# Optimization experiments

Measured on AMD Instinct MI355X. Metric: run time of the kernel, lower is better.

The kernel has to match this reference:

```python
import jax, jax.numpy as jnp
import numpy as np

PATCH = 16


def setup_inputs() -> dict:
    key = jax.random.key(0)
    x = jax.random.normal(key, (256, 3, 224, 224), dtype=jnp.float32)
    return {"x": x}


def reference(x):
    P = PATCH
    B, C, Hi, Wi = x.shape
    h, w = Hi // P, Wi // P  # grid rows (h) and cols (w)
    # 'b c (h p1) (w p2) -> b w h p1 p2 c'
    patches = x.reshape(B, C, h, P, w, P).transpose(0, 4, 2, 3, 5, 1)  # (B, w, h, p1, p2, C)
    # center_rotate: transpose p1<->p2 for patches with grid col j in [w/3, 2w/3]
    # and grid row k in [h/3, 2h/3] (original skips j < W/3 or j > 2W/3, same for k)
    jw = jnp.arange(w)
    kh = jnp.arange(h)
    mw = (jw >= w / 3) & (jw <= 2 * w / 3)
    mh = (kh >= h / 3) & (kh <= 2 * h / 3)
    mask = (mw[:, None] & mh[None, :])[None, :, :, None, None, None]  # (1, w, h, 1, 1, 1)
    rot = jnp.where(mask, jnp.swapaxes(patches, 3, 4), patches)  # (B, w, h, a3, a4, C)
    # 'b w h p2 p1 c -> b c (h p2) (w p1)': axis3 is read as p2 (inner height),
    # axis4 as p1 (inner width) -- i.e. every patch gets transposed on reassembly,
    # so center patches (transposed twice) come back in original orientation.
    out = rot.transpose(0, 5, 2, 3, 1, 4).reshape(B, C, h * P, w * P)
    return out
```

## Files before the change

kernel.cpp:

```cpp
#include <hip/hip_runtime.h>


#define W4 56
#define IMG_F4 12544
#define LDS_S 84
#define NT 512

__global__ __launch_bounds__(NT) void patch_rotate_kernel(
    const float4* __restrict__ x, float4* __restrict__ out) {
  const int bc = blockIdx.x;
  const float4* __restrict__ xs = x + (size_t)bc * IMG_F4;
  float4* __restrict__ os = out + (size_t)bc * IMG_F4;
  const int tid = threadIdx.x;

  __shared__ float ldsT[5 * 16 * LDS_S];

  for (int i = tid; i < 1600; i += NT) {
    const int sr = i / 20;
    const int c4 = i % 20;
    const float4 v = xs[(80 + sr) * W4 + 20 + c4];
    const int ks = sr >> 4;
    const int ar = sr & 15;
    const int jl = c4 >> 2;
    const int ac0 = (c4 & 3) << 2;
    float* p = ldsT + (ks * 16 + ac0) * LDS_S + jl * 16 + ar;
    p[0 * LDS_S] = v.x;
    p[1 * LDS_S] = v.y;
    p[2 * LDS_S] = v.z;
    p[3 * LDS_S] = v.w;
  }

  for (int i = tid; i < 4480; i += NT) os[i] = xs[i];
  for (int i = 8960 + tid; i < IMG_F4; i += NT) os[i] = xs[i];
  for (int i = tid; i < 2880; i += NT) {
    const int r = i / 36;
    const int cc = i % 36;
    const int c4 = cc < 20 ? cc : cc + 20;
    const int idx = (80 + r) * W4 + c4;
    os[idx] = xs[idx];
  }

  __syncthreads();

  for (int i = tid; i < 1600; i += NT) {
    const int orr = i / 20;
    const int c4 = i % 20;
    const float* p = ldsT + orr * LDS_S + c4 * 4;
    float4 v;
    v.x = p[0]; v.y = p[1]; v.z = p[2]; v.w = p[3];
    os[(80 + orr) * W4 + 20 + c4] = v;
  }
}

extern "C" void kernel_launch(void* const* d_in, const int* in_sizes, int n_in,
                              void* d_out, int out_size, void* d_ws, size_t ws_size,
                              hipStream_t stream) {
  const float* x = (const float*)d_in[0];
  float* out = (float*)d_out;
  patch_rotate_kernel<<<768, NT, 0, stream>>>((const float4*)x, (float4*)out);
}
```

Before: 275.4 us.

## Replace per-image LDS block kernel with flat per-float4 elementwise gather kernel

Drops the one-block-per-image design, which staged the center 5x5 patch region through shared memory. It launches one thread per output float4 instead. Non-center elements are copied with nontemporal vector loads and stores. Center elements gather four strided scalars directly from global memory to perform the transpose. This raises the grid size and removes the barrier and LDS traffic, at the cost of uncoalesced strided reads in the center region and more integer index math per thread.

```diff
diff --git a/kernel.cpp b/kernel.cpp
--- a/kernel.cpp
+++ b/kernel.cpp
@@ -1,54 +1,40 @@
 #include <hip/hip_runtime.h>
 
 
+#define HH 224
+#define WW 224
 #define W4 56
-#define IMG_F4 12544
-#define LDS_S 84
-#define NT 512
 
-__global__ __launch_bounds__(NT) void patch_rotate_kernel(
-    const float4* __restrict__ x, float4* __restrict__ out) {
-  const int bc = blockIdx.x;
-  const float4* __restrict__ xs = x + (size_t)bc * IMG_F4;
-  float4* __restrict__ os = out + (size_t)bc * IMG_F4;
-  const int tid = threadIdx.x;
+typedef float vf4 __attribute__((ext_vector_type(4)));
 
-  __shared__ float ldsT[5 * 16 * LDS_S];
+__global__ __launch_bounds__(256) void patch_rotate_kernel(
+    const float* __restrict__ x, float* __restrict__ out, int n4) {
+  int idx = blockIdx.x * blockDim.x + threadIdx.x;
+  if (idx >= n4) return;
 
-  for (int i = tid; i < 1600; i += NT) {
-    const int sr = i / 20;
-    const int c4 = i % 20;
-    const float4 v = xs[(80 + sr) * W4 + 20 + c4];
-    const int ks = sr >> 4;
-    const int ar = sr & 15;
-    const int jl = c4 >> 2;
-    const int ac0 = (c4 & 3) << 2;
-    float* p = ldsT + (ks * 16 + ac0) * LDS_S + jl * 16 + ar;
-    p[0 * LDS_S] = v.x;
-    p[1 * LDS_S] = v.y;
-    p[2 * LDS_S] = v.z;
-    p[3 * LDS_S] = v.w;
-  }
+  int bc   = idx / (HH * W4);
+  int rem  = idx % (HH * W4);
+  int row  = rem / W4;
+  int col4 = rem % W4;
 
-  for (int i = tid; i < 4480; i += NT) os[i] = xs[i];
-  for (int i = 8960 + tid; i < IMG_F4; i += NT) os[i] = xs[i];
-  for (int i = tid; i < 2880; i += NT) {
-    const int r = i / 36;
-    const int cc = i % 36;
-    const int c4 = cc < 20 ? cc : cc + 20;
-    const int idx = (80 + r) * W4 + c4;
-    os[idx] = xs[idx];
-  }
+  int k = row >> 4;
+  int j = col4 >> 2;
 
-  __syncthreads();
+  bool center = (j >= 5) & (j <= 9) & (k >= 5) & (k <= 9);
 
-  for (int i = tid; i < 1600; i += NT) {
-    const int orr = i / 20;
-    const int c4 = i % 20;
-    const float* p = ldsT + orr * LDS_S + c4 * 4;
-    float4 v;
-    v.x = p[0]; v.y = p[1]; v.z = p[2]; v.w = p[3];
-    os[(80 + orr) * W4 + 20 + c4] = v;
+  if (!center) {
+    vf4 v = __builtin_nontemporal_load((const vf4*)x + idx);
+    __builtin_nontemporal_store(v, (vf4*)out + idx);
+  } else {
+    int a3  = row & 15;
+    int a4b = (col4 & 3) << 2;
+    int base = (bc * HH + (k << 4)) * WW + (j << 4) + a3;
+    vf4 v;
+    v.x = x[base + (a4b + 0) * WW];
+    v.y = x[base + (a4b + 1) * WW];
+    v.z = x[base + (a4b + 2) * WW];
+    v.w = x[base + (a4b + 3) * WW];
+    *((vf4*)out + idx) = v;
   }
 }
 
@@ -57,5 +43,8 @@
                               hipStream_t stream) {
   const float* x = (const float*)d_in[0];
   float* out = (float*)d_out;
-  patch_rotate_kernel<<<768, NT, 0, stream>>>((const float4*)x, (float4*)out);
+  int n4 = out_size / 4;
+  int threads = 256;
+  int blocks = (n4 + threads - 1) / threads;
+  patch_rotate_kernel<<<blocks, threads, 0, stream>>>(x, out, n4);
 }
```

Measured after the change: 257.2 us. -6.6%, faster.
